# Kernel tuning notes

Measured on AMD Instinct MI355X. Metric: run time of the kernel, lower is better.

The kernel has to match this reference:

```python
import jax, jax.numpy as jnp
import numpy as np

N_NODES = 100000
N_EDGES = 1000000
IN_DIM = 128
H = [64, 64, 64, 64, 128]
OUT_DIM = 64
K = 3  # TAGConv default hops
BN_EPS = 1e-5


def _gcn_norm(src, dst, num_nodes):
    # symmetric normalization D^{-1/2} A D^{-1/2}, no self loops (PyG TAGConv default)
    deg = jax.ops.segment_sum(jnp.ones(src.shape[0], jnp.float32), dst, num_segments=num_nodes)
    dis = jnp.where(deg > 0, jax.lax.rsqrt(jnp.maximum(deg, 1.0)), 0.0)
    return dis[src] * dis[dst]  # [E]


def _tagconv(x, src, dst, norm, Ws, b, num_nodes):
    # Ws: [K+1, in, out]; out = sum_k (A_hat^k x) @ W_k + b
    out = x @ Ws[0]
    h = x
    for k in range(1, K + 1):
        h = jax.ops.segment_sum(h[src] * norm[:, None], dst, num_segments=num_nodes)
        out = out + h @ Ws[k]
    return out + b


def setup_inputs() -> dict:
    key = jax.random.key(0)
    ks = jax.random.split(key, 16)
    s = 0.05
    x = jax.random.normal(ks[0], (N_NODES, IN_DIM), jnp.float32)
    edge_index = jax.random.randint(ks[1], (2, N_EDGES), 0, N_NODES, dtype=jnp.int64)
    return {
        "x": x,
        "edge_index": edge_index,
        "bn_gamma": jnp.ones((IN_DIM,), jnp.float32),
        "bn_beta": jnp.zeros((IN_DIM,), jnp.float32),
        "W1": jax.random.normal(ks[2], (IN_DIM, H[0]), jnp.float32) * s,
        "b1": jnp.zeros((H[0],), jnp.float32),
        "tag1_W": jax.random.normal(ks[3], (K + 1, H[0], H[1]), jnp.float32) * s,
        "tag1_b": jnp.zeros((H[1],), jnp.float32),
        "W2": jax.random.normal(ks[4], (H[1], H[2]), jnp.float32) * s,
        "b2": jnp.zeros((H[2],), jnp.float32),
        "tag2_W": jax.random.normal(ks[5], (K + 1, H[2], H[3]), jnp.float32) * s,
        "tag2_b": jnp.zeros((H[3],), jnp.float32),
        "W3": jax.random.normal(ks[6], (H[3] + IN_DIM, H[4]), jnp.float32) * s,
        "b3": jnp.zeros((H[4],), jnp.float32),
        "W4": jax.random.normal(ks[7], (H[4], OUT_DIM), jnp.float32) * s,
        "b4": jnp.zeros((OUT_DIM,), jnp.float32),
    }


def reference(x, edge_index, bn_gamma, bn_beta, W1, b1, tag1_W, tag1_b,
              W2, b2, tag2_W, tag2_b, W3, b3, W4, b4):
    gelu = lambda t: jax.nn.gelu(t, approximate=False)  # torch GELU default (erf)
    src, dst = edge_index[0], edge_index[1]
    norm = _gcn_norm(src, dst, N_NODES)

    # BatchNorm over nodes (training-mode batch stats, biased variance)
    mean = jnp.mean(x, axis=0)
    var = jnp.mean((x - mean) ** 2, axis=0)
    x_norm = (x - mean) * jax.lax.rsqrt(var + BN_EPS) * bn_gamma + bn_beta

    h = gelu(x_norm @ W1 + b1)
    h = gelu(_tagconv(h, src, dst, norm, tag1_W, tag1_b, N_NODES))
    h = gelu(h @ W2 + b2)
    h = gelu(_tagconv(h, src, dst, norm, tag2_W, tag2_b, N_NODES))
    a = jnp.concatenate([x, h], axis=1)
    a = gelu(a @ W3 + b3)
    return a @ W4 + b4
```

## Files before the change

kernel.cpp:

```cpp
#include <hip/hip_runtime.h>
#include <stdint.h>

typedef unsigned short u16;
typedef unsigned int   u32;
typedef __attribute__((ext_vector_type(8))) short short8;
typedef __attribute__((ext_vector_type(4))) float float4v;

#define DEV __device__ __forceinline__

DEV float bf2f(u16 u){ return __uint_as_float(((u32)u)<<16); }
DEV u16 f2bf(float f){
  u32 u = __float_as_uint(f);
  u32 r = u + 0x7fffu + ((u>>16)&1u);
  return (u16)(r>>16);
}
DEV float gelu_f(float x){ return 0.5f*x*(1.0f + erff(x*0.70710678118654752f)); }
DEV float ldext(const void* b, size_t i, int f32){
  return f32 ? ((const float*)b)[i] : bf2f(((const u16*)b)[i]);
}
DEV int ld_src(const int* ei, int e, int E, int m64){ return m64 ? ei[2*e]     : ei[e]; }
DEV int ld_dst(const int* ei, int e, int E, int m64){ return m64 ? ei[2*(E+e)] : ei[E+e]; }
DEV int swz(int k, int n){
  return (((k>>5)*4 + (n>>4))*64 + ((((k>>3)&3)<<4) | (n&15)))*8 + (k&7);
}

__global__ __launch_bounds__(256) void detect_types(const int* __restrict__ ei,
                                                    const u16* __restrict__ xw,
                                                    int* __restrict__ flags){
  __shared__ int a64, insane;
  int t = threadIdx.x;
  if (t==0){ a64=0; insane=0; }
  __syncthreads();
  int l=0;
  for (int i=t; i<4096; i+=256) l |= ei[2*i+1];
  if (l) atomicOr(&a64, 1);
  int c=0;
  for (int i=t; i<2048; i+=256){
    u16 lo = xw[2*i];
    int e8 = (lo>>7)&0xff;
    if (e8!=0 && (e8<90 || e8>160)) c++;
  }
  atomicAdd(&insane, c);
  __syncthreads();
  if (t==0){ flags[0] = a64?0:1; flags[1] = (insane>256)?1:0; }
}

__global__ __launch_bounds__(256) void econv(const int* __restrict__ ei,
                                             const int* __restrict__ flags,
                                             int* __restrict__ s32, int* __restrict__ d32, int E){
  int m64 = flags[0];
  for (int e = blockIdx.x*256 + threadIdx.x; e < E; e += gridDim.x*256){
    s32[e] = ld_src(ei, e, E, m64);
    d32[e] = ld_dst(ei, e, E, m64);
  }
}

__global__ __launch_bounds__(256) void xconv(const void* __restrict__ x,
                                             const int* __restrict__ flags,
                                             u16* __restrict__ xbf, int total8){
  if (!flags[1]) return;
  for (size_t i = (size_t)(blockIdx.x*256 + threadIdx.x)*8; i < (size_t)total8*8;
       i += (size_t)gridDim.x*256*8){
    const float* xf = (const float*)x + i;
    float4 a = *(const float4*)xf;
    float4 b = *(const float4*)(xf+4);
    u16 o[8];
    o[0]=f2bf(a.x); o[1]=f2bf(a.y); o[2]=f2bf(a.z); o[3]=f2bf(a.w);
    o[4]=f2bf(b.x); o[5]=f2bf(b.y); o[6]=f2bf(b.z); o[7]=f2bf(b.w);
    *(uint4*)(xbf + i) = *(uint4*)o;
  }
}

__global__ __launch_bounds__(256) void bn_stats(const void* __restrict__ x,
                                                const int* __restrict__ flags,
                                                float* __restrict__ sums, int N){
  __shared__ float red[16][128];
  int f32  = flags[1];
  int tid  = threadIdx.x;
  int col  = tid & 15;
  int rsub = tid >> 4;
  float s8[8], q8[8];
  #pragma unroll
  for (int j=0;j<8;j++){ s8[j]=0.f; q8[j]=0.f; }
  for (int r = blockIdx.x*16 + rsub; r < N; r += gridDim.x*16){
    float f[8];
    if (f32){
      const float* xp = (const float*)x + (size_t)r*128 + col*8;
      float4 A = *(const float4*)xp;
      float4 B = *(const float4*)(xp+4);
      f[0]=A.x; f[1]=A.y; f[2]=A.z; f[3]=A.w;
      f[4]=B.x; f[5]=B.y; f[6]=B.z; f[7]=B.w;
    } else {
      const u16* xp = (const u16*)x + (size_t)r*128 + col*8;
      uint4 u = *(const uint4*)xp;
      f[0]=bf2f((u16)(u.x&0xffffu)); f[1]=bf2f((u16)(u.x>>16));
      f[2]=bf2f((u16)(u.y&0xffffu)); f[3]=bf2f((u16)(u.y>>16));
      f[4]=bf2f((u16)(u.z&0xffffu)); f[5]=bf2f((u16)(u.z>>16));
      f[6]=bf2f((u16)(u.w&0xffffu)); f[7]=bf2f((u16)(u.w>>16));
    }
    #pragma unroll
    for (int j=0;j<8;j++){ s8[j]+=f[j]; q8[j]+=f[j]*f[j]; }
  }
  #pragma unroll
  for (int j=0;j<8;j++) red[rsub][col*8+j] = s8[j];
  __syncthreads();
  if (tid < 128){
    float t=0.f;
    #pragma unroll
    for (int i=0;i<16;i++) t += red[i][tid];
    atomicAdd(&sums[tid], t);
  }
  __syncthreads();
  #pragma unroll
  for (int j=0;j<8;j++) red[rsub][col*8+j] = q8[j];
  __syncthreads();
  if (tid < 128){
    float t=0.f;
    #pragma unroll
    for (int i=0;i<16;i++) t += red[i][tid];
    atomicAdd(&sums[128+tid], t);
  }
}

__global__ __launch_bounds__(256) void edge_count(const int* __restrict__ d32, int E, int N,
                                                  int* __restrict__ cnt){
  int part = blockIdx.x & 7;
  int lo = (int)((long)N*part/8), hi = (int)((long)N*(part+1)/8);
  int bid = blockIdx.x >> 3;
  int nb  = gridDim.x >> 3;
  for (int e = bid*256 + threadIdx.x; e < E; e += nb*256){
    int d = d32[e];
    if (d >= lo && d < hi) atomicAdd(&cnt[d], 1);
  }
}

#define SCAN_CHUNK 1024
__global__ __launch_bounds__(256) void scan_a(const int* __restrict__ cnt, int N,
                                              int* __restrict__ ofs, int* __restrict__ blksum,
                                              float* __restrict__ dis){
  __shared__ int lds[256];
  int t = threadIdx.x;
  int base = blockIdx.x*SCAN_CHUNK + t*4;
  int v[4];
  #pragma unroll
  for (int i=0;i<4;i++){ int idx=base+i; v[i] = (idx<N) ? cnt[idx] : 0; }
  #pragma unroll
  for (int i=0;i<4;i++){ int idx=base+i; if (idx<N) dis[idx] = v[i]>0 ? rsqrtf((float)v[i]) : 0.f; }
  int tsum = v[0]+v[1]+v[2]+v[3];
  lds[t] = tsum; __syncthreads();
  for (int off=1; off<256; off<<=1){
    int add = (t>=off) ? lds[t-off] : 0;
    __syncthreads();
    lds[t] += add;
    __syncthreads();
  }
  int run = lds[t] - tsum;
  #pragma unroll
  for (int i=0;i<4;i++){ int idx=base+i; if (idx<N) ofs[idx]=run; run += v[i]; }
  if (t==255) blksum[blockIdx.x] = lds[255];
}

__global__ void scan_b(const int* __restrict__ blksum, int nblk, int* __restrict__ blkoff){
  if (threadIdx.x==0 && blockIdx.x==0){
    int r=0;
    for (int i=0;i<nblk;i++){ blkoff[i]=r; r+=blksum[i]; }
  }
}

__global__ __launch_bounds__(256) void scan_c(int* __restrict__ ofs, const int* __restrict__ blkoff,
                                              int N, int E, int* __restrict__ cur){
  int i = blockIdx.x*256 + threadIdx.x;
  if (i < N){
    int v = ofs[i] + blkoff[i/SCAN_CHUNK];
    ofs[i] = v; cur[i] = v;
  }
  if (i==0) ofs[N] = E;
}

__global__ __launch_bounds__(256) void edge_scatter(const int* __restrict__ s32,
                                                    const int* __restrict__ d32, int E, int N,
                                                    const float* __restrict__ dis,
                                                    int* __restrict__ cur, int2* __restrict__ epack){
  int part = blockIdx.x & 7;
  int lo = (int)((long)N*part/8), hi = (int)((long)N*(part+1)/8);
  int bid = blockIdx.x >> 3;
  int nb  = gridDim.x >> 3;
  for (int e = bid*256 + threadIdx.x; e < E; e += nb*256){
    int d = d32[e];
    if (d < lo || d >= hi) continue;
    int s = s32[e];
    if ((unsigned)s >= (unsigned)N) continue;
    int p = atomicAdd(&cur[d], 1);
    if ((unsigned)p < (unsigned)E){
      int2 pk; pk.x = s; pk.y = __float_as_int(dis[s]*dis[d]);
      epack[p] = pk;
    }
  }
}

struct PrepOut {
  u16 *W1p,*Wt1,*Wt2,*W2p,*W3a,*W3b,*W4p;
  float *b1p,*bt1,*bt2,*b2p,*b3a,*b3b,*b4p;
};

#define PREP_TOTAL 78272

__global__ __launch_bounds__(256) void prep(const float* __restrict__ sums, float invN,
    const int* __restrict__ flags,
    const void* g, const void* be,
    const void* W1, const void* b1,
    const void* t1W, const void* t1b,
    const void* W2, const void* b2,
    const void* t2W, const void* t2b,
    const void* W3, const void* b3,
    const void* W4, const void* b4,
    PrepOut o)
{
  int f32 = flags[1];
  int idx = blockIdx.x*256 + threadIdx.x;
  if (idx >= PREP_TOTAL) return;
  auto scale_shift = [&](int f, float& sc, float& sh){
    float m   = sums[f]*invN;
    float var = sums[128+f]*invN - m*m;
    sc = ldext(g,f,f32) * rsqrtf(var + 1e-5f);
    sh = ldext(be,f,f32) - m*sc;
  };
  if (idx < 8192){
    int k=idx>>6, n=idx&63; float sc,sh; scale_shift(k,sc,sh);
    o.W1p[swz(k,n)] = f2bf(sc*ldext(W1,idx,f32)); return;
  }
  idx -= 8192;
  if (idx < 64){
    float acc = ldext(b1,idx,f32);
    for (int f=0; f<128; f++){ float sc,sh; scale_shift(f,sc,sh); acc += sh*ldext(W1,f*64+idx,f32); }
    o.b1p[idx]=acc; return;
  }
  idx -= 64;
  if (idx < 16384){ int k=idx>>6,n=idx&63; o.Wt1[swz(k,n)]=f2bf(ldext(t1W,idx,f32)); return; }  idx -= 16384;
  if (idx < 64)   { o.bt1[idx]=ldext(t1b,idx,f32); return; }  idx -= 64;
  if (idx < 16384){ int k=idx>>6,n=idx&63; o.Wt2[swz(k,n)]=f2bf(ldext(t2W,idx,f32)); return; }  idx -= 16384;
  if (idx < 64)   { o.bt2[idx]=ldext(t2b,idx,f32); return; }  idx -= 64;
  if (idx < 4096) { int k=idx>>6,n=idx&63; o.W2p[swz(k,n)]=f2bf(ldext(W2,idx,f32));  return; }  idx -= 4096;
  if (idx < 64)   { o.b2p[idx]=ldext(b2,idx,f32);  return; }  idx -= 64;
  if (idx < 12288){ int k=idx>>6,n=idx&63; o.W3a[swz(k,n)]=f2bf(ldext(W3,(size_t)k*128+n,f32));    return; }  idx -= 12288;
  if (idx < 64)   { o.b3a[idx]=ldext(b3,idx,f32);  return; }  idx -= 64;
  if (idx < 12288){ int k=idx>>6,n=idx&63; o.W3b[swz(k,n)]=f2bf(ldext(W3,(size_t)k*128+64+n,f32)); return; }  idx -= 12288;
  if (idx < 64)   { o.b3b[idx]=ldext(b3,64+idx,f32); return; } idx -= 64;
  if (idx < 8192) { int k=idx>>6,n=idx&63; o.W4p[swz(k,n)]=f2bf(ldext(W4,idx,f32));  return; }
  else            { o.b4p[idx-8192]=ldext(b4,idx-8192,f32); }
}

struct KD { const u16* p[8]; int ld[8]; };

template<int KS,int OUTMODE>
__global__ __launch_bounds__(256,2) void gemm_mfma(
    KD d, const u16* __restrict__ Wsw, const float* __restrict__ bias,
    void* __restrict__ out, int ldo, int ocol,
    int N, const int* __restrict__ flags, long xdelta, u32 xmask)
{
  constexpr int LBYTES = OUTMODE ? 128*68*4 : 128*72*2;
  __shared__ __align__(16) char lds[LBYTES];
  if (xmask && !flags[1]){
    #pragma unroll
    for (int t=0;t<KS;t++) if (xmask & (1u<<t)) d.p[t] += xdelta;
  }
  int tid = threadIdx.x, w = tid>>6, l = tid&63;
  int rlo = l&15, kq = l>>4;
  int row0b = blockIdx.x*128;
  int row0  = row0b + w*32;

  short8 Bf[KS][4];
  #pragma unroll
  for (int t=0;t<KS;t++)
    #pragma unroll
    for (int c=0;c<4;c++)
      Bf[t][c] = *(const short8*)(Wsw + ((t*4+c)*64 + l)*8);

  float4v a0[4], a1[4];
  #pragma unroll
  for (int c=0;c<4;c++){
    a0[c].x=0;a0[c].y=0;a0[c].z=0;a0[c].w=0;
    a1[c].x=0;a1[c].y=0;a1[c].z=0;a1[c].w=0;
  }

  #pragma unroll
  for (int t=0;t<KS;t++){
    const u16* ap = d.p[t]; int ld = d.ld[t];
    short8 A0 = *(const short8*)(ap + (size_t)(row0+rlo)*ld + kq*8);
    short8 A1 = *(const short8*)(ap + (size_t)(row0+16+rlo)*ld + kq*8);
    #pragma unroll
    for (int c=0;c<4;c++){
      a0[c] = __builtin_amdgcn_mfma_f32_16x16x32_bf16(A0, Bf[t][c], a0[c], 0,0,0);
      a1[c] = __builtin_amdgcn_mfma_f32_16x16x32_bf16(A1, Bf[t][c], a1[c], 0,0,0);
    }
  }

  float bv[4];
  #pragma unroll
  for (int c=0;c<4;c++) bv[c] = bias[c*16 + rlo];

  int nrow = N - row0b; if (nrow > 128) nrow = 128; if (nrow < 0) nrow = 0;

  if (OUTMODE==0){
    u16* s = (u16*)lds;
    #pragma unroll
    for (int c=0;c<4;c++){
      int col = c*16 + rlo;
      #pragma unroll
      for (int r=0;r<4;r++){
        s[(w*32 +      kq*4 + r)*72 + col] = f2bf(gelu_f(a0[c][r] + bv[c]));
        s[(w*32 + 16 + kq*4 + r)*72 + col] = f2bf(gelu_f(a1[c][r] + bv[c]));
      }
    }
    __syncthreads();
    u16* ob = (u16*)out + (size_t)row0b*ldo + ocol;
    for (int i=tid; i<nrow*8; i+=256){
      int r = i>>3, cc = (i&7)<<3;
      *(uint4*)(ob + (size_t)r*ldo + cc) = *(const uint4*)(s + r*72 + cc);
    }
  } else {
    int f32o = flags[1];
    if (f32o){
      float* sf = (float*)lds;
      #pragma unroll
      for (int c=0;c<4;c++){
        int col = c*16 + rlo;
        #pragma unroll
        for (int r=0;r<4;r++){
          float v0 = a0[c][r] + bv[c]; float v1 = a1[c][r] + bv[c];
          sf[(w*32 +      kq*4 + r)*68 + col] = isfinite(v0)?v0:777.0f;
          sf[(w*32 + 16 + kq*4 + r)*68 + col] = isfinite(v1)?v1:777.0f;
        }
      }
      __syncthreads();
      float* ob = (float*)out + (size_t)row0b*64;
      for (int i=tid; i<nrow*16; i+=256){
        int r = i>>4, cc = (i&15)<<2;
        *(uint4*)(ob + (size_t)r*64 + cc) = *(const uint4*)(sf + r*68 + cc);
      }
    } else {
      u16* s = (u16*)lds;
      #pragma unroll
      for (int c=0;c<4;c++){
        int col = c*16 + rlo;
        #pragma unroll
        for (int r=0;r<4;r++){
          float v0 = a0[c][r] + bv[c]; float v1 = a1[c][r] + bv[c];
          s[(w*32 +      kq*4 + r)*72 + col] = f2bf(isfinite(v0)?v0:777.0f);
          s[(w*32 + 16 + kq*4 + r)*72 + col] = f2bf(isfinite(v1)?v1:777.0f);
        }
      }
      __syncthreads();
      u16* ob = (u16*)out + (size_t)row0b*64;
      for (int i=tid; i<nrow*8; i+=256){
        int r = i>>3, cc = (i&7)<<3;
        *(uint4*)(ob + (size_t)r*64 + cc) = *(const uint4*)(s + r*72 + cc);
      }
    }
  }
}

__global__ __launch_bounds__(256) void spmm(const int* __restrict__ rofs,
    const int2* __restrict__ epack,
    const u16* __restrict__ hin, u16* __restrict__ hout, int N)
{
  int lane = threadIdx.x & 63;
  int wv   = (int)((blockIdx.x*256 + threadIdx.x) >> 6);
  int sub  = lane >> 3;
  int f8   = (lane & 7) * 8;
  int row  = wv*8 + sub;
  bool rok = row < N;
  int beg = rok ? rofs[row]   : 0;
  int end = rok ? rofs[row+1] : 0;

  float acc[8];
  #pragma unroll
  for (int j=0;j<8;j++) acc[j]=0.f;

  int e = beg;
  int2 pk; pk.x = 0; pk.y = 0;
  if (e < end) pk = epack[e];

  while (__any(e < end)){
    bool act = e < end;
    int   s = act ? pk.x : 0;
    float w = act ? __int_as_float(pk.y) : 0.f;
    if ((u32)s >= (u32)N){ s = 0; w = 0.f; }
    uint4 v = *(const uint4*)(hin + (size_t)s*64 + f8);
    int e1 = e + 1;
    if (e1 < end) pk = epack[e1];
    acc[0] += w*__uint_as_float(v.x<<16);
    acc[1] += w*__uint_as_float(v.x&0xffff0000u);
    acc[2] += w*__uint_as_float(v.y<<16);
    acc[3] += w*__uint_as_float(v.y&0xffff0000u);
    acc[4] += w*__uint_as_float(v.z<<16);
    acc[5] += w*__uint_as_float(v.z&0xffff0000u);
    acc[6] += w*__uint_as_float(v.w<<16);
    acc[7] += w*__uint_as_float(v.w&0xffff0000u);
    e = e1;
  }

  if (rok){
    u16 o[8];
    #pragma unroll
    for (int j=0;j<8;j++) o[j]=f2bf(acc[j]);
    *(uint4*)(hout + (size_t)row*64 + f8) = *(uint4*)o;
  }
}

extern "C" void kernel_launch(void* const* d_in, const int* in_sizes, int n_in,
                              void* d_out, int out_size, void* d_ws, size_t ws_size,
                              hipStream_t stream)
{
  const void* x   = d_in[0];
  const int*  ei  = (const int*)d_in[1];
  const void* gam = d_in[2];  const void* bet = d_in[3];
  const void* W1  = d_in[4];  const void* b1  = d_in[5];
  const void* t1W = d_in[6];  const void* t1b = d_in[7];
  const void* W2  = d_in[8];  const void* b2  = d_in[9];
  const void* t2W = d_in[10]; const void* t2b = d_in[11];
  const void* W3  = d_in[12]; const void* b3  = d_in[13];
  const void* W4  = d_in[14]; const void* b4  = d_in[15];

  const int N = in_sizes[0]/128;
  const int E = in_sizes[1]/2;

  char* p = (char*)d_ws;
  auto carve = [&](size_t bytes)->void*{
    void* r = (void*)p;
    p += (bytes + 255) & ~(size_t)255;
    return r;
  };
  int*   row_cnt = (int*)  carve((size_t)N*4);
  float* bnsums  = (float*)carve(256*4);
  int*   flags   = (int*)  carve(256);
  size_t zero_span = (size_t)((char*)flags + 256 - (char*)row_cnt);
  int*   row_ofs = (int*)  carve((size_t)(N+1)*4);
  int*   blksum  = (int*)  carve(1024*4);
  int*   blkoff  = (int*)  carve(1024*4);
  float* dis     = (float*)carve((size_t)N*4);
  int*   src32   = (int*)  carve((size_t)E*4);
  int*   dst32   = (int*)  carve((size_t)E*4);
  int2*  epack   = (int2*) carve((size_t)E*8);
  PrepOut po;
  po.W1p=(u16*)carve(8192*2);   po.b1p=(float*)carve(64*4);
  po.Wt1=(u16*)carve(16384*2);  po.bt1=(float*)carve(64*4);
  po.Wt2=(u16*)carve(16384*2);  po.bt2=(float*)carve(64*4);
  po.W2p=(u16*)carve(4096*2);   po.b2p=(float*)carve(64*4);
  po.W3a=(u16*)carve(12288*2);  po.b3a=(float*)carve(64*4);
  po.W3b=(u16*)carve(12288*2);  po.b3b=(float*)carve(64*4);
  po.W4p=(u16*)carve(8192*2);   po.b4p=(float*)carve(64*4);
  u16* xbf  = (u16*)carve((size_t)N*128*2);
  u16* buf0 = (u16*)carve((size_t)N*64*2);
  u16* buf1 = (u16*)carve((size_t)N*64*2);
  u16* buf2 = (u16*)carve((size_t)N*64*2);
  u16* buf3 = (u16*)carve((size_t)N*64*2);
  u16* buf4 = (u16*)carve((size_t)N*64*2);
  carve(64*1024);
  u16* Ka   = buf0;

  size_t needed = (size_t)(p - (char*)d_ws);
  if (needed > ws_size){
    hipMemsetAsync(d_out, 0, (size_t)out_size*2, stream);
    return;
  }

  long xdelta = (const u16*)x - xbf;

  const int nchunk = (N + SCAN_CHUNK-1)/SCAN_CHUNK;
  const int rblk   = (N + 255)/256;
  const int gblk   = (N + 127)/128;
  const int sblk   = (N + 31)/32;

  hipMemsetAsync(row_cnt, 0, zero_span, stream);

  detect_types<<<1, 256, 0, stream>>>(ei, (const u16*)x, flags);
  econv       <<<2048,256,0,stream>>>(ei, flags, src32, dst32, E);
  bn_stats    <<<512,256,0, stream>>>(x, flags, bnsums, N);
  edge_count  <<<2048,256,0,stream>>>(dst32, E, N, row_cnt);
  scan_a      <<<nchunk,256,0,stream>>>(row_cnt, N, row_ofs, blksum, dis);
  scan_b      <<<1,  64, 0, stream>>>(blksum, nchunk, blkoff);
  scan_c      <<<rblk,256,0, stream>>>(row_ofs, blkoff, N, E, row_cnt);
  edge_scatter<<<2048,256,0,stream>>>(src32, dst32, E, N, dis, row_cnt, epack);
  prep        <<<(PREP_TOTAL+255)/256, 256, 0, stream>>>(bnsums, 1.0f/(float)N, flags,
                 gam, bet, W1, b1, t1W, t1b, W2, b2, t2W, t2b, W3, b3, W4, b4, po);
  xconv       <<<4096,256,0,stream>>>(x, flags, xbf, N*16);

  KD dx;   for (int t=0;t<4;t++){ dx.p[t]  = xbf + t*32;  dx.ld[t]=128; }
           for (int t=4;t<8;t++){ dx.p[t]  = xbf;         dx.ld[t]=128; }
  KD dcat; { u16* bs[4]={buf0,buf1,buf2,buf3};
             for (int t=0;t<8;t++){ dcat.p[t]=bs[t>>1]+(t&1)*32; dcat.ld[t]=64; } }
  KD d3;   for (int t=0;t<4;t++){ d3.p[t]  = xbf + t*32;  d3.ld[t]=128; }
           d3.p[4]=buf4; d3.ld[4]=64; d3.p[5]=buf4+32; d3.ld[5]=64;
           d3.p[6]=buf4; d3.ld[6]=64; d3.p[7]=buf4;    d3.ld[7]=64;
  KD d4;   for (int t=0;t<4;t++){ d4.p[t]  = Ka + t*32;   d4.ld[t]=128; }
           for (int t=4;t<8;t++){ d4.p[t]  = Ka;          d4.ld[t]=128; }

  gemm_mfma<4,0><<<gblk,256,0,stream>>>(dx, po.W1p, po.b1p, buf0,64,0, N, flags, xdelta, 0xFu);
  spmm<<<sblk,256,0,stream>>>(row_ofs, epack, buf0, buf1, N);
  spmm<<<sblk,256,0,stream>>>(row_ofs, epack, buf1, buf2, N);
  spmm<<<sblk,256,0,stream>>>(row_ofs, epack, buf2, buf3, N);
  gemm_mfma<8,0><<<gblk,256,0,stream>>>(dcat, po.Wt1, po.bt1, buf4,64,0, N, flags, 0, 0);
  { KD dl2; for (int t=0;t<8;t++){ dl2.p[t]=buf4+(t&1)*32; dl2.ld[t]=64; }
    gemm_mfma<2,0><<<gblk,256,0,stream>>>(dl2, po.W2p, po.b2p, buf0,64,0, N, flags, 0, 0); }
  spmm<<<sblk,256,0,stream>>>(row_ofs, epack, buf0, buf1, N);
  spmm<<<sblk,256,0,stream>>>(row_ofs, epack, buf1, buf2, N);
  spmm<<<sblk,256,0,stream>>>(row_ofs, epack, buf2, buf3, N);
  gemm_mfma<8,0><<<gblk,256,0,stream>>>(dcat, po.Wt2, po.bt2, buf4,64,0, N, flags, 0, 0);
  gemm_mfma<6,0><<<gblk,256,0,stream>>>(d3, po.W3a, po.b3a, Ka,128,0,  N, flags, xdelta, 0xFu);
  gemm_mfma<6,0><<<gblk,256,0,stream>>>(d3, po.W3b, po.b3b, Ka,128,64, N, flags, xdelta, 0xFu);
  gemm_mfma<4,1><<<gblk,256,0,stream>>>(d4, po.W4p, po.b4p, d_out,64,0, N, flags, 0, 0);
}
```

Measured before the change: 535.4 us.

## Fuse edge count into index conversion and x bf16 cast into BN stats

After: 494.4 us. 7.6% less time.

```diff
diff --git a/kernel.cpp b/kernel.cpp
--- a/kernel.cpp
+++ b/kernel.cpp
@@ -45,35 +45,28 @@
   if (t==0){ flags[0] = a64?0:1; flags[1] = (insane>256)?1:0; }
 }
 
-__global__ __launch_bounds__(256) void econv(const int* __restrict__ ei,
-                                             const int* __restrict__ flags,
-                                             int* __restrict__ s32, int* __restrict__ d32, int E){
+__global__ __launch_bounds__(256) void econv_count(const int* __restrict__ ei,
+                                                   const int* __restrict__ flags,
+                                                   int* __restrict__ s32, int* __restrict__ d32,
+                                                   int* __restrict__ rankc, int* __restrict__ cnt8,
+                                                   int E, int N){
   int m64 = flags[0];
+  int c = (int)(blockIdx.x & 7);
+  int* cnt = cnt8 + (size_t)c*N;
   for (int e = blockIdx.x*256 + threadIdx.x; e < E; e += gridDim.x*256){
-    s32[e] = ld_src(ei, e, E, m64);
-    d32[e] = ld_dst(ei, e, E, m64);
-  }
-}
-
-__global__ __launch_bounds__(256) void xconv(const void* __restrict__ x,
-                                             const int* __restrict__ flags,
-                                             u16* __restrict__ xbf, int total8){
-  if (!flags[1]) return;
-  for (size_t i = (size_t)(blockIdx.x*256 + threadIdx.x)*8; i < (size_t)total8*8;
-       i += (size_t)gridDim.x*256*8){
-    const float* xf = (const float*)x + i;
-    float4 a = *(const float4*)xf;
-    float4 b = *(const float4*)(xf+4);
-    u16 o[8];
-    o[0]=f2bf(a.x); o[1]=f2bf(a.y); o[2]=f2bf(a.z); o[3]=f2bf(a.w);
-    o[4]=f2bf(b.x); o[5]=f2bf(b.y); o[6]=f2bf(b.z); o[7]=f2bf(b.w);
-    *(uint4*)(xbf + i) = *(uint4*)o;
+    int s = ld_src(ei, e, E, m64);
+    int d = ld_dst(ei, e, E, m64);
+    s32[e] = s; d32[e] = d;
+    int r = 0;
+    if ((unsigned)d < (unsigned)N) r = atomicAdd(&cnt[d], 1);
+    rankc[e] = (r<<3) | c;
   }
 }
 
 __global__ __launch_bounds__(256) void bn_stats(const void* __restrict__ x,
                                                 const int* __restrict__ flags,
-                                                float* __restrict__ sums, int N){
+                                                float* __restrict__ sums,
+                                                u16* __restrict__ xbf, int N){
   __shared__ float red[16][128];
   int f32  = flags[1];
   int tid  = threadIdx.x;
@@ -90,6 +83,10 @@
       float4 B = *(const float4*)(xp+4);
       f[0]=A.x; f[1]=A.y; f[2]=A.z; f[3]=A.w;
       f[4]=B.x; f[5]=B.y; f[6]=B.z; f[7]=B.w;
+      u16 o[8];
+      #pragma unroll
+      for (int j=0;j<8;j++) o[j] = f2bf(f[j]);
+      *(uint4*)(xbf + (size_t)r*128 + col*8) = *(uint4*)o;
     } else {
       const u16* xp = (const u16*)x + (size_t)r*128 + col*8;
       uint4 u = *(const uint4*)xp;
@@ -122,20 +119,8 @@
   }
 }
 
-__global__ __launch_bounds__(256) void edge_count(const int* __restrict__ d32, int E, int N,
-                                                  int* __restrict__ cnt){
-  int part = blockIdx.x & 7;
-  int lo = (int)((long)N*part/8), hi = (int)((long)N*(part+1)/8);
-  int bid = blockIdx.x >> 3;
-  int nb  = gridDim.x >> 3;
-  for (int e = bid*256 + threadIdx.x; e < E; e += nb*256){
-    int d = d32[e];
-    if (d >= lo && d < hi) atomicAdd(&cnt[d], 1);
-  }
-}
-
 #define SCAN_CHUNK 1024
-__global__ __launch_bounds__(256) void scan_a(const int* __restrict__ cnt, int N,
+__global__ __launch_bounds__(256) void scan_a(const int* __restrict__ cnt8, int N,
                                               int* __restrict__ ofs, int* __restrict__ blksum,
                                               float* __restrict__ dis){
   __shared__ int lds[256];
@@ -143,7 +128,14 @@
   int base = blockIdx.x*SCAN_CHUNK + t*4;
   int v[4];
   #pragma unroll
-  for (int i=0;i<4;i++){ int idx=base+i; v[i] = (idx<N) ? cnt[idx] : 0; }
+  for (int i=0;i<4;i++){
+    int idx = base+i; int s = 0;
+    if (idx < N){
+      #pragma unroll
+      for (int c=0;c<8;c++) s += cnt8[(size_t)c*N + idx];
+    }
+    v[i] = s;
+  }
   #pragma unroll
   for (int i=0;i<4;i++){ int idx=base+i; if (idx<N) dis[idx] = v[i]>0 ? rsqrtf((float)v[i]) : 0.f; }
   int tsum = v[0]+v[1]+v[2]+v[3];
@@ -164,37 +156,40 @@
   if (threadIdx.x==0 && blockIdx.x==0){
     int r=0;
     for (int i=0;i<nblk;i++){ blkoff[i]=r; r+=blksum[i]; }
+    blkoff[nblk]=r;
   }
 }
 
 __global__ __launch_bounds__(256) void scan_c(int* __restrict__ ofs, const int* __restrict__ blkoff,
-                                              int N, int E, int* __restrict__ cur){
+                                              const int* __restrict__ cnt8, int* __restrict__ base8,
+                                              int N, int nchunk){
   int i = blockIdx.x*256 + threadIdx.x;
   if (i < N){
     int v = ofs[i] + blkoff[i/SCAN_CHUNK];
-    ofs[i] = v; cur[i] = v;
-  }
-  if (i==0) ofs[N] = E;
+    ofs[i] = v;
+    int run = v;
+    #pragma unroll
+    for (int c=0;c<8;c++){ base8[(size_t)c*N + i] = run; run += cnt8[(size_t)c*N + i]; }
+  }
+  if (i==0) ofs[N] = blkoff[nchunk];
 }
 
 __global__ __launch_bounds__(256) void edge_scatter(const int* __restrict__ s32,
-                                                    const int* __restrict__ d32, int E, int N,
+                                                    const int* __restrict__ d32,
+                                                    const int* __restrict__ rankc,
+                                                    const int* __restrict__ base8,
                                                     const float* __restrict__ dis,
-                                                    int* __restrict__ cur, int2* __restrict__ epack){
-  int part = blockIdx.x & 7;
-  int lo = (int)((long)N*part/8), hi = (int)((long)N*(part+1)/8);
-  int bid = blockIdx.x >> 3;
-  int nb  = gridDim.x >> 3;
-  for (int e = bid*256 + threadIdx.x; e < E; e += nb*256){
+                                                    int2* __restrict__ epack, int E, int N){
+  for (int e = blockIdx.x*256 + threadIdx.x; e < E; e += gridDim.x*256){
     int d = d32[e];
-    if (d < lo || d >= hi) continue;
-    int s = s32[e];
-    if ((unsigned)s >= (unsigned)N) continue;
-    int p = atomicAdd(&cur[d], 1);
-    if ((unsigned)p < (unsigned)E){
-      int2 pk; pk.x = s; pk.y = __float_as_int(dis[s]*dis[d]);
-      epack[p] = pk;
-    }
+    if ((unsigned)d >= (unsigned)N) continue;
+    int rc = rankc[e];
+    int p  = base8[(size_t)(rc&7)*N + d] + (rc>>3);
+    int s  = s32[e];
+    int2 pk;
+    if ((unsigned)s < (unsigned)N){ pk.x = s; pk.y = __float_as_int(dis[s]*dis[d]); }
+    else                          { pk.x = 0; pk.y = 0; }
+    if ((unsigned)p < (unsigned)E) epack[p] = pk;
   }
 }
 
@@ -431,16 +426,18 @@
     p += (bytes + 255) & ~(size_t)255;
     return r;
   };
-  int*   row_cnt = (int*)  carve((size_t)N*4);
+  int*   cnt8    = (int*)  carve((size_t)N*8*4);
   float* bnsums  = (float*)carve(256*4);
   int*   flags   = (int*)  carve(256);
-  size_t zero_span = (size_t)((char*)flags + 256 - (char*)row_cnt);
+  size_t zero_span = (size_t)((char*)flags + 256 - (char*)cnt8);
   int*   row_ofs = (int*)  carve((size_t)(N+1)*4);
   int*   blksum  = (int*)  carve(1024*4);
-  int*   blkoff  = (int*)  carve(1024*4);
+  int*   blkoff  = (int*)  carve(1032*4);
   float* dis     = (float*)carve((size_t)N*4);
+  int*   base8   = (int*)  carve((size_t)N*8*4);
   int*   src32   = (int*)  carve((size_t)E*4);
   int*   dst32   = (int*)  carve((size_t)E*4);
+  int*   rankc   = (int*)  carve((size_t)E*4);
   int2*  epack   = (int2*) carve((size_t)E*8);
   PrepOut po;
   po.W1p=(u16*)carve(8192*2);   po.b1p=(float*)carve(64*4);
@@ -472,19 +469,17 @@
   const int gblk   = (N + 127)/128;
   const int sblk   = (N + 31)/32;
 
-  hipMemsetAsync(row_cnt, 0, zero_span, stream);
+  hipMemsetAsync(cnt8, 0, zero_span, stream);
 
   detect_types<<<1, 256, 0, stream>>>(ei, (const u16*)x, flags);
-  econv       <<<2048,256,0,stream>>>(ei, flags, src32, dst32, E);
-  bn_stats    <<<512,256,0, stream>>>(x, flags, bnsums, N);
-  edge_count  <<<2048,256,0,stream>>>(dst32, E, N, row_cnt);
-  scan_a      <<<nchunk,256,0,stream>>>(row_cnt, N, row_ofs, blksum, dis);
+  econv_count <<<2048,256,0,stream>>>(ei, flags, src32, dst32, rankc, cnt8, E, N);
+  bn_stats    <<<512,256,0, stream>>>(x, flags, bnsums, xbf, N);
+  scan_a      <<<nchunk,256,0,stream>>>(cnt8, N, row_ofs, blksum, dis);
   scan_b      <<<1,  64, 0, stream>>>(blksum, nchunk, blkoff);
-  scan_c      <<<rblk,256,0, stream>>>(row_ofs, blkoff, N, E, row_cnt);
-  edge_scatter<<<2048,256,0,stream>>>(src32, dst32, E, N, dis, row_cnt, epack);
+  scan_c      <<<rblk,256,0, stream>>>(row_ofs, blkoff, cnt8, base8, N, nchunk);
+  edge_scatter<<<2048,256,0,stream>>>(src32, dst32, rankc, base8, dis, epack, E, N);
   prep        <<<(PREP_TOTAL+255)/256, 256, 0, stream>>>(bnsums, 1.0f/(float)N, flags,
                  gam, bet, W1, b1, t1W, t1b, W2, b2, t2W, t2b, W3, b3, W4, b4, po);
-  xconv       <<<4096,256,0,stream>>>(x, flags, xbf, N*16);
 
   KD dx;   for (int t=0;t<4;t++){ dx.p[t]  = xbf + t*32;  dx.ld[t]=128; }
            for (int t=4;t<8;t++){ dx.p[t]  = xbf;         dx.ld[t]=128; }
```
